# Performance work log

Hardware: AMD Instinct MI355X
Metric: run time of the kernel (lower is better)

## Reference

```python
import jax, jax.numpy as jnp
import numpy as np
from math import sqrt

B, IN_C, OUT_C, H, W, WDIM, K = 16, 512, 512, 64, 64, 512, 3
EPS = 1e-8
LRELU_SLOPE = 0.2


def setup_inputs() -> dict:
    key = jax.random.key(0)
    ks = jax.random.split(key, 5)
    return {
        "x": jax.random.normal(ks[0], (B, IN_C, H, W), dtype=jnp.float32),
        "w": jax.random.normal(ks[1], (B, WDIM), dtype=jnp.float32),
        "noise": jax.random.normal(ks[2], (B, 1, H, W), dtype=jnp.float32),
        "linear_w": jax.random.normal(ks[3], (IN_C, WDIM), dtype=jnp.float32),
        "linear_b": jnp.ones((IN_C,), dtype=jnp.float32),
        "conv_w": jax.random.normal(ks[4], (OUT_C, IN_C, K, K), dtype=jnp.float32),
        "scale_noise": jnp.zeros((OUT_C,), dtype=jnp.float32),
        "bias": jnp.zeros((OUT_C,), dtype=jnp.float32),
    }


def reference(x, w, noise, linear_w, linear_b, conv_w, scale_noise, bias):
    # EqualizerStraights: equalized-lr linear, scale = 1/sqrt(w_dim)
    s = w @ (linear_w * (1.0 / sqrt(WDIM))).T + linear_b  # [b, in_c]
    # Weight_Demod: equalized conv weight, scale = 1/sqrt(in_c*k*k)
    base_w = conv_w * (1.0 / sqrt(IN_C * K * K))  # [out, in, k, k]
    weights = base_w[None] * s[:, None, :, None, None]  # [b, out, in, k, k]
    sigma_inv = jax.lax.rsqrt(
        jnp.sum(weights * weights, axis=(2, 3, 4), keepdims=True) + EPS)
    weights = weights * sigma_inv

    def conv1(xi, wi):  # xi [in,h,w], wi [out,in,k,k]
        return jax.lax.conv_general_dilated(
            xi[None], wi, window_strides=(1, 1), padding="SAME",
            dimension_numbers=("NCHW", "OIHW", "NCHW"))[0]

    y = jax.vmap(conv1)(x, weights)  # [b, out, h, w]
    y = y + scale_noise[None, :, None, None] * noise
    return jax.nn.leaky_relu(y + bias[None, :, None, None], negative_slope=LRELU_SLOPE)
```

## Files before the change

### kernel.cpp

```cpp
#include <hip/hip_runtime.h>
#include <hip/hip_bf16.h>
#include <stdint.h>

typedef __bf16 bf16_t;
typedef __bf16 bf16x8 __attribute__((ext_vector_type(8)));
typedef short short8 __attribute__((ext_vector_type(8)));
typedef float f32x4 __attribute__((ext_vector_type(4)));
typedef float f32x16 __attribute__((ext_vector_type(16)));

#define RS512  0.044194173824159216f
#define RS4608 0.014731391274719739f

__global__ void k_style(const float* __restrict__ w, const float* __restrict__ lw,
                        const float* __restrict__ lb, float* __restrict__ s) {
  int b = blockIdx.y;
  int c = blockIdx.x * 256 + threadIdx.x;
  const float4* wr = (const float4*)(w + b * 512);
  const float4* lr = (const float4*)(lw + (size_t)c * 512);
  float acc = 0.f;
#pragma unroll 4
  for (int d = 0; d < 128; ++d) {
    float4 a = wr[d], q = lr[d];
    acc += a.x * q.x + a.y * q.y + a.z * q.z + a.w * q.w;
  }
  s[b * 512 + c] = acc * RS512 + lb[c];
}

__global__ void k_wprep(const float* __restrict__ cw, float* __restrict__ wsq,
                        bf16_t* __restrict__ bwf, f32x4* __restrict__ zb) {
  if (blockIdx.x == 0) zb[threadIdx.x] = (f32x4)0.f;
  int idx = blockIdx.x * 256 + threadIdx.x;
  int o = idx >> 9, i = idx & 511;
  float v[9];
  float ss = 0.f;
#pragma unroll
  for (int t = 0; t < 9; ++t) {
    float x = cw[(size_t)idx * 9 + t] * RS4608;
    v[t] = x;
    ss += x * x;
  }
  wsq[idx] = ss;
  int c32 = i >> 5, fo = o >> 5, ks = (i >> 4) & 1;
  int ln = (o & 31) + ((i >> 3) & 1) * 32;
#pragma unroll
  for (int t = 0; t < 9; ++t) {
    size_t e = ((size_t)(((t * 16 + c32) * 16 + fo) * 2 + ks) << 9) + ln * 8 + (i & 7);
    bwf[e] = (bf16_t)v[t];
  }
}

__global__ void k_sigma(const float* __restrict__ s, const float* __restrict__ wsq,
                        float* __restrict__ sinv) {
  __shared__ float s2[512];
  int b = blockIdx.y;
  int o = blockIdx.x * 256 + threadIdx.x;
  for (int i = threadIdx.x; i < 512; i += 256) {
    float v = s[b * 512 + i];
    s2[i] = v * v;
  }
  __syncthreads();
  const float4* qr = (const float4*)(wsq + (size_t)o * 512);
  float acc = 0.f;
#pragma unroll 4
  for (int d = 0; d < 128; ++d) {
    float4 q = qr[d];
    acc += q.x * s2[4 * d] + q.y * s2[4 * d + 1] + q.z * s2[4 * d + 2] + q.w * s2[4 * d + 3];
  }
  sinv[b * 512 + o] = rsqrtf(acc + 1e-8f);
}

__global__ void k_xt(const float* __restrict__ x, const float* __restrict__ s,
                     bf16_t* __restrict__ xt) {
  int ic = blockIdx.x, h = blockIdx.y, b = blockIdx.z;
  __shared__ __align__(16) bf16_t tile[8192];
  int t = threadIdx.x;
  int wcol = t & 63;
  int g = t >> 6;
#pragma unroll
  for (int blk = 0; blk < 4; ++blk) {
    int grp = blk * 4 + g;
    bf16x8 vec;
#pragma unroll
    for (int k = 0; k < 8; ++k) {
      int i = ic * 128 + grp * 8 + k;
      float v = x[(((size_t)b * 512 + i) * 64 + h) * 64 + wcol] * s[b * 512 + i];
      vec[k] = (bf16_t)v;
    }
    *(bf16x8*)((char*)tile + grp * 1024 + wcol * 16) = vec;
  }
  __syncthreads();
  char* dst = (char*)xt + ((((size_t)b * 64 + h) * 16 + ic * 4) << 12) + g * 1024 + wcol * 16;
#pragma unroll
  for (int j = 0; j < 4; ++j) {
    bf16x8 v = *(bf16x8*)((char*)tile + (j * 4 + g) * 1024 + wcol * 16);
    *(bf16x8*)(dst + j * 4096) = v;
  }
}

#define AS1 __attribute__((address_space(1)))
#define AS3 __attribute__((address_space(3)))

__device__ __forceinline__ void gl16(const void* g, void* l) {
  __builtin_amdgcn_global_load_lds((const AS1 void*)g, (AS3 void*)l, 16, 0, 0);
}

#define VMCNT(n) asm volatile("s_waitcnt vmcnt(" #n ")" ::: "memory")

#define XT0 4096u

__global__ __launch_bounds__(512, 4) void k_conv(
    const char* __restrict__ wsb,
    const bf16_t* __restrict__ bwf,
    const float* __restrict__ sinv, const float* __restrict__ noise,
    const float* __restrict__ snz, const float* __restrict__ bias,
    float* __restrict__ out) {
  __shared__ __align__(16) char lds[51200];

  const int t = threadIdx.x;
  const int rq = blockIdx.x;
  const int OY = blockIdx.y;
  const int b = blockIdx.z;
  const int h0 = rq * 4;
  const int lane = t & 63;
  const int wv = t >> 6;
  const int wm = wv & 1;
  const int wn = wv >> 1;

  f32x16 acc[2][2] = {};
  bf16x8 wA[4], wB[4];

  uint32_t xsoff[3], xdst[3], xsel[3];
#pragma unroll
  for (int k = 0; k < 3; ++k) {
    int slot = wv * 3 + k, row = slot >> 2, q = slot & 3;
    int gr = h0 - 1 + row;
    int valid = ((unsigned)gr < 64u) ? 1 : 0;
    uint32_t so = valid ? (XT0 + (uint32_t)b * 4194304u + (uint32_t)gr * 65536u +
                           (uint32_t)q * 1024u)
                        : 0u;
    xsoff[k] = __builtin_amdgcn_readfirstlane(so);
    xdst[k] = __builtin_amdgcn_readfirstlane((uint32_t)(1024 + row * 4096 + q * 1024));
    xsel[k] = __builtin_amdgcn_readfirstlane((uint32_t)valid);
  }

  auto stX = [&](int k, uint32_t cxoff, int xb) {
    uint32_t co = xsel[k] ? cxoff : 0u;
    gl16(wsb + xsoff[k] + co + (size_t)(lane * 16), lds + xdst[k] + (uint32_t)(xb * 24576));
  };

  const size_t wbase0 = ((size_t)(OY * 4 + wm * 2)) << 11;
  auto loadW = [&](int tap, int c, bf16x8* d) {
    const char* p = (const char*)bwf + wbase0 + (((size_t)(tap * 16 + c)) << 15) +
                    (size_t)(lane * 16);
#pragma unroll
    for (int f = 0; f < 2; ++f)
#pragma unroll
      for (int ks = 0; ks < 2; ++ks)
        d[f * 2 + ks] = *(const bf16x8*)(p + f * 2048 + ks * 1024);
  };

  const uint32_t pXbase =
      (uint32_t)(1024 + wn * 4096 + (lane >> 5) * 1024 + (lane & 31) * 16);
  const bool cl = (lane & 31) == 0;
  const bool cr = (lane & 31) == 31;

#define CTAP(J, XB, AF)                                                        \
  {                                                                            \
    const int ky = (J) / 3, kx = (J) % 3;                                      \
    __builtin_amdgcn_s_setprio(1);                                             \
    _Pragma("unroll") for (int nf = 0; nf < 2; ++nf) {                         \
      bf16x8 b0, b1;                                                           \
      {                                                                        \
        short8 xv = *(const short8*)(lds + pXbase +                            \
            (uint32_t)((XB) * 24576 + ky * 4096 + nf * 512 + (kx - 1) * 16));  \
        if (kx == 0 && nf == 0) xv = cl ? (short8)0 : xv;                      \
        if (kx == 2 && nf == 1) xv = cr ? (short8)0 : xv;                      \
        b0 = __builtin_bit_cast(bf16x8, xv);                                   \
      }                                                                        \
      {                                                                        \
        short8 xv = *(const short8*)(lds + pXbase +                            \
            (uint32_t)((XB) * 24576 + ky * 4096 + 2048 + nf * 512 +            \
                       (kx - 1) * 16));                                        \
        if (kx == 0 && nf == 0) xv = cl ? (short8)0 : xv;                      \
        if (kx == 2 && nf == 1) xv = cr ? (short8)0 : xv;                      \
        b1 = __builtin_bit_cast(bf16x8, xv);                                   \
      }                                                                        \
      _Pragma("unroll") for (int f = 0; f < 2; ++f) {                          \
        acc[f][nf] = __builtin_amdgcn_mfma_f32_32x32x16_bf16(                  \
            AF[f * 2 + 0], b0, acc[f][nf], 0, 0, 0);                           \
        acc[f][nf] = __builtin_amdgcn_mfma_f32_32x32x16_bf16(                  \
            AF[f * 2 + 1], b1, acc[f][nf], 0, 0, 0);                           \
      }                                                                        \
    }                                                                          \
    __builtin_amdgcn_s_setprio(0);                                             \
  }

#define CHUNK(C, XB, P, LAST)                                                  \
  {                                                                            \
    _Pragma("unroll") for (int j = 0; j < 9; ++j) {                            \
      if (!(LAST) && j < 3) stX(j, (uint32_t)(((C) + 1) * 4096), (XB) ^ 1);    \
      if (j < 8) {                                                             \
        if (((j + (P)) & 1) == 0) loadW(j + 1, (C), wB);                       \
        else loadW(j + 1, (C), wA);                                            \
      } else if (!(LAST)) {                                                    \
        if (((j + (P)) & 1) == 0) loadW(0, (C) + 1, wB);                       \
        else loadW(0, (C) + 1, wA);                                            \
      }                                                                        \
      if (((j + (P)) & 1) == 0) CTAP(j, (XB), wA)                              \
      else CTAP(j, (XB), wB)                                                   \
    }                                                                          \
    if (!(LAST)) { VMCNT(4); __builtin_amdgcn_s_barrier(); }                   \
  }

#pragma unroll
  for (int k = 0; k < 3; ++k) stX(k, 0u, 0);
  loadW(0, 0, wA);
  __syncthreads();

#pragma unroll 1
  for (int ci = 0; ci < 7; ++ci) {
    const int c = ci * 2;
    CHUNK(c, 0, 0, 0);
    CHUNK(c + 1, 1, 1, 0);
  }
  CHUNK(14, 0, 0, 0);
  CHUNK(15, 1, 1, 1);

  const float* sb = sinv + b * 512;
  const int colb = lane & 31;
  const int rq4 = (lane >> 5) * 4;
  const int prow = h0 + wn;
  float nz0 = noise[(size_t)b * 4096 + prow * 64 + colb];
  float nz1 = noise[(size_t)b * 4096 + prow * 64 + 32 + colb];
#pragma unroll
  for (int f = 0; f < 2; ++f) {
#pragma unroll
    for (int r = 0; r < 16; ++r) {
      int o = OY * 128 + wm * 64 + f * 32 + (r & 3) + 8 * (r >> 2) + rq4;
      float sv = sb[o];
      float nw = snz[o];
      float bv = bias[o];
      float* orow = out + (((size_t)b * 512 + o) * 64 + prow) * 64;
      float v0 = acc[f][0][r] * sv + nw * nz0 + bv;
      float v1 = acc[f][1][r] * sv + nw * nz1 + bv;
      orow[colb] = v0 > 0.f ? v0 : 0.2f * v0;
      orow[32 + colb] = v1 > 0.f ? v1 : 0.2f * v1;
    }
  }
}

extern "C" void kernel_launch(void* const* d_in, const int* in_sizes, int n_in,
                              void* d_out, int out_size, void* d_ws, size_t ws_size,
                              hipStream_t stream) {
  const float* x     = (const float*)d_in[0];
  const float* w     = (const float*)d_in[1];
  const float* noise = (const float*)d_in[2];
  const float* lw    = (const float*)d_in[3];
  const float* lb    = (const float*)d_in[4];
  const float* cw    = (const float*)d_in[5];
  const float* snz   = (const float*)d_in[6];
  const float* bias  = (const float*)d_in[7];
  float* out = (float*)d_out;

  char* ws = (char*)d_ws;
  char*   zbuf = ws;
  bf16_t* xt   = (bf16_t*)(ws + 4096);
  bf16_t* bwf  = (bf16_t*)(ws + 67112960);
  float*  s    = (float*)(ws + 71831552);
  float*  sinv = (float*)(ws + 71864320);
  float*  wsq  = (float*)(ws + 71897088);

  k_style<<<dim3(2, 16), 256, 0, stream>>>(w, lw, lb, s);
  k_wprep<<<dim3(1024), 256, 0, stream>>>(cw, wsq, bwf, (f32x4*)zbuf);
  k_sigma<<<dim3(2, 16), 256, 0, stream>>>(s, wsq, sinv);
  k_xt<<<dim3(4, 64, 16), 256, 0, stream>>>(x, s, xt);
  k_conv<<<dim3(16, 4, 16), 512, 0, stream>>>(ws, bwf, sinv, noise, snz, bias, out);
}
```

Measured before the change: 360.5 us.

## Stage conv weight tiles through LDS with triple-buffered async loads per tap

Weight fragments were previously loaded from global memory straight into registers with double buffering. They are now streamed via global_load_lds into a three-slot LDS ring, one slab per tap, prefetched two taps ahead, with per-tap vmcnt waits and a barrier before each tap's MFMAs. The aim is to cut register pressure and take global-load latency off the MFMA critical path, and the shared slab also means each block fetches a given weight tile once instead of every wave loading it. In exchange LDS grows to 74752 bytes per block, which may cut occupancy below the declared 4 blocks, and a workgroup barrier is now taken every tap instead of every chunk.

```diff
diff --git a/kernel.cpp b/kernel.cpp
--- a/kernel.cpp
+++ b/kernel.cpp
@@ -105,16 +105,16 @@
 }
 
 #define VMCNT(n) asm volatile("s_waitcnt vmcnt(" #n ")" ::: "memory")
+#define BAR __builtin_amdgcn_s_barrier()
 
 #define XT0 4096u
 
 __global__ __launch_bounds__(512, 4) void k_conv(
-    const char* __restrict__ wsb,
-    const bf16_t* __restrict__ bwf,
+    const char* __restrict__ wsb, const bf16_t* __restrict__ bwf,
     const float* __restrict__ sinv, const float* __restrict__ noise,
     const float* __restrict__ snz, const float* __restrict__ bias,
     float* __restrict__ out) {
-  __shared__ __align__(16) char lds[51200];
+  __shared__ __align__(16) char lds[74752];
 
   const int t = threadIdx.x;
   const int rq = blockIdx.x;
@@ -127,7 +127,6 @@
   const int wn = wv >> 1;
 
   f32x16 acc[2][2] = {};
-  bf16x8 wA[4], wB[4];
 
   uint32_t xsoff[3], xdst[3], xsel[3];
 #pragma unroll
@@ -139,7 +138,7 @@
                            (uint32_t)q * 1024u)
                         : 0u;
     xsoff[k] = __builtin_amdgcn_readfirstlane(so);
-    xdst[k] = __builtin_amdgcn_readfirstlane((uint32_t)(1024 + row * 4096 + q * 1024));
+    xdst[k] = __builtin_amdgcn_readfirstlane((uint32_t)(24576 + row * 4096 + q * 1024));
     xsel[k] = __builtin_amdgcn_readfirstlane((uint32_t)valid);
   }
 
@@ -148,25 +147,26 @@
     gl16(wsb + xsoff[k] + co + (size_t)(lane * 16), lds + xdst[k] + (uint32_t)(xb * 24576));
   };
 
-  const size_t wbase0 = ((size_t)(OY * 4 + wm * 2)) << 11;
-  auto loadW = [&](int tap, int c, bf16x8* d) {
-    const char* p = (const char*)bwf + wbase0 + (((size_t)(tap * 16 + c)) << 15) +
-                    (size_t)(lane * 16);
-#pragma unroll
-    for (int f = 0; f < 2; ++f)
-#pragma unroll
-      for (int ks = 0; ks < 2; ++ks)
-        d[f * 2 + ks] = *(const bf16x8*)(p + f * 2048 + ks * 1024);
+  const char* wgsrc = (const char*)bwf + OY * 8192 + wv * 1024 + lane * 16;
+  auto stW = [&](uint32_t srcoff, int slab) {
+    gl16(wgsrc + srcoff, lds + slab * 8192 + (wv << 10));
   };
 
+  const uint32_t woff = (uint32_t)((wm * 2) * 2048 + (lane << 4));
   const uint32_t pXbase =
-      (uint32_t)(1024 + wn * 4096 + (lane >> 5) * 1024 + (lane & 31) * 16);
+      (uint32_t)(24576 + wn * 4096 + (lane >> 5) * 1024 + (lane & 31) * 16);
   const bool cl = (lane & 31) == 0;
   const bool cr = (lane & 31) == 31;
 
-#define CTAP(J, XB, AF)                                                        \
+#define CTAP(J, XB)                                                            \
   {                                                                            \
     const int ky = (J) / 3, kx = (J) % 3;                                      \
+    bf16x8 af[4];                                                              \
+    _Pragma("unroll") for (int f = 0; f < 2; ++f)                              \
+        _Pragma("unroll") for (int ks = 0; ks < 2; ++ks)                       \
+            af[f * 2 + ks] = *(const bf16x8*)(                                 \
+                lds + (uint32_t)(((J) % 3) * 8192) + woff +                    \
+                (uint32_t)(f * 2048 + ks * 1024));                             \
     __builtin_amdgcn_s_setprio(1);                                             \
     _Pragma("unroll") for (int nf = 0; nf < 2; ++nf) {                         \
       bf16x8 b0, b1;                                                           \
@@ -187,44 +187,54 @@
       }                                                                        \
       _Pragma("unroll") for (int f = 0; f < 2; ++f) {                          \
         acc[f][nf] = __builtin_amdgcn_mfma_f32_32x32x16_bf16(                  \
-            AF[f * 2 + 0], b0, acc[f][nf], 0, 0, 0);                           \
+            af[f * 2 + 0], b0, acc[f][nf], 0, 0, 0);                           \
         acc[f][nf] = __builtin_amdgcn_mfma_f32_32x32x16_bf16(                  \
-            AF[f * 2 + 1], b1, acc[f][nf], 0, 0, 0);                           \
+            af[f * 2 + 1], b1, acc[f][nf], 0, 0, 0);                           \
       }                                                                        \
     }                                                                          \
     __builtin_amdgcn_s_setprio(0);                                             \
   }
 
-#define CHUNK(C, XB, P, LAST)                                                  \
+#define PHASE(CWB, CXB, JC, LAST, XB)                                          \
   {                                                                            \
-    _Pragma("unroll") for (int j = 0; j < 9; ++j) {                            \
-      if (!(LAST) && j < 3) stX(j, (uint32_t)(((C) + 1) * 4096), (XB) ^ 1);    \
-      if (j < 8) {                                                             \
-        if (((j + (P)) & 1) == 0) loadW(j + 1, (C), wB);                       \
-        else loadW(j + 1, (C), wA);                                            \
-      } else if (!(LAST)) {                                                    \
-        if (((j + (P)) & 1) == 0) loadW(0, (C) + 1, wB);                       \
-        else loadW(0, (C) + 1, wA);                                            \
-      }                                                                        \
-      if (((j + (P)) & 1) == 0) CTAP(j, (XB), wA)                              \
-      else CTAP(j, (XB), wB)                                                   \
+    if ((JC) + 2 <= 8) stW((CWB) + (uint32_t)((JC) + 2) * 524288u, ((JC) + 2) % 3); \
+    else if (!(LAST)) stW((CWB) + 32768u + (uint32_t)((JC) - 7) * 524288u, ((JC) + 2) % 3); \
+    if (!(LAST) && (JC) < 3) stX((JC), (CXB), (XB) ^ 1);                       \
+    if (LAST) {                                                                \
+      if ((JC) <= 6) { VMCNT(2); }                                             \
+      else if ((JC) == 7) { VMCNT(1); }                                        \
+      else { VMCNT(0); }                                                       \
+    } else {                                                                   \
+      if ((JC) == 0 || (JC) == 4) { VMCNT(3); }                                \
+      else if ((JC) == 1 || (JC) == 3) { VMCNT(4); }                           \
+      else if ((JC) == 2) { VMCNT(5); }                                        \
+      else { VMCNT(2); }                                                       \
     }                                                                          \
-    if (!(LAST)) { VMCNT(4); __builtin_amdgcn_s_barrier(); }                   \
+    __builtin_amdgcn_s_barrier();                                              \
+    CTAP((JC), (XB));                                                          \
   }
 
 #pragma unroll
   for (int k = 0; k < 3; ++k) stX(k, 0u, 0);
-  loadW(0, 0, wA);
-  __syncthreads();
-
+  stW(0u, 0);
+  stW(524288u, 1);
+  VMCNT(0); BAR;
+
+  uint32_t cwb = 0, cxb = 4096;
 #pragma unroll 1
   for (int ci = 0; ci < 7; ++ci) {
-    const int c = ci * 2;
-    CHUNK(c, 0, 0, 0);
-    CHUNK(c + 1, 1, 1, 0);
-  }
-  CHUNK(14, 0, 0, 0);
-  CHUNK(15, 1, 1, 1);
+#pragma unroll
+    for (int jc = 0; jc < 9; ++jc) PHASE(cwb, cxb, jc, 0, 0);
+    cwb += 32768u; cxb += 4096u;
+#pragma unroll
+    for (int jc = 0; jc < 9; ++jc) PHASE(cwb, cxb, jc, 0, 1);
+    cwb += 32768u; cxb += 4096u;
+  }
+#pragma unroll
+  for (int jc = 0; jc < 9; ++jc) PHASE(cwb, cxb, jc, 0, 0);
+  cwb += 32768u;
+#pragma unroll
+  for (int jc = 0; jc < 9; ++jc) PHASE(cwb, 0u, jc, 1, 1);
 
   const float* sb = sinv + b * 512;
   const int colb = lane & 31;
```

Result: faster. 333.6 us (-7.5%).
